# Optimization experiments

Measured on AMD Instinct MI355X. Metric: run time of the kernel, lower is better.

## Reference

```python
import jax, jax.numpy as jnp
import numpy as np

NUM_HEADS = 16

def setup_inputs() -> dict:
    key = jax.random.key(0)
    k1, k2, k3 = jax.random.split(key, 3)
    B, S, D = 2, 2048, 1024
    return {
        "hidden_states": jax.random.normal(k1, (B, S, D), dtype=jnp.float32),
        "W_attn": jax.random.normal(k2, (D, 3 * D), dtype=jnp.float32) * 0.02,
        "b_attn": jnp.zeros((3 * D,), dtype=jnp.float32),
        "W_proj": jax.random.normal(k3, (D, D), dtype=jnp.float32) * 0.02,
        "b_proj": jnp.zeros((D,), dtype=jnp.float32),
    }

def reference(hidden_states, W_attn, b_attn, W_proj, b_proj):
    B, S, D = hidden_states.shape
    H = NUM_HEADS
    hd = D // H
    # qkv projection (Conv1D == addmm): [B,S,3D]
    qkv = hidden_states @ W_attn + b_attn
    q, k, v = jnp.split(qkv, 3, axis=-1)
    # split heads -> [B,H,S,hd]
    def split_heads(t):
        return t.reshape(B, S, H, hd).transpose(0, 2, 1, 3)
    q, k, v = split_heads(q), split_heads(k), split_heads(v)
    # scaled QK^T: [B,H,S,S]
    scores = jnp.einsum('bhqd,bhkd->bhqk', q, k) / jnp.asarray(hd ** 0.5, dtype=q.dtype)
    causal = jnp.tril(jnp.ones((S, S), dtype=bool))
    mask_value = jnp.finfo(scores.dtype).min
    scores = jnp.where(causal, scores, mask_value)
    probs = jax.nn.softmax(scores, axis=-1)  # attn_pdrop=0 -> no dropout
    out = jnp.einsum('bhqk,bhkd->bhqd', probs, v)
    # merge heads -> [B,S,D]
    out = out.transpose(0, 2, 1, 3).reshape(B, S, D)
    out = out @ W_proj + b_proj  # resid_pdrop=0 -> no dropout
    return out
```

## Files before the change

### kernel.cpp

```cpp
#include <hip/hip_runtime.h>
#include <math.h>

typedef __attribute__((ext_vector_type(8))) short bf16x8;
typedef __attribute__((ext_vector_type(4))) short bf16x4;
typedef __attribute__((ext_vector_type(4))) float f32x4;

#define MFMA16(a, b, c) __builtin_amdgcn_mfma_f32_16x16x32_bf16(a, b, c, 0, 0, 0)

#define GLOAD_LDS16(g, l)                                                        \
    __builtin_amdgcn_global_load_lds(                                            \
        (const __attribute__((address_space(1))) void*)(g),                      \
        (__attribute__((address_space(3))) void*)(l), 16, 0, 0)

#define SBAR() __builtin_amdgcn_s_barrier()
#define PRIO(x) __builtin_amdgcn_s_setprio(x)
#define VMW6 asm volatile("s_waitcnt vmcnt(6)" ::: "memory")
#define VMW4 asm volatile("s_waitcnt vmcnt(4)" ::: "memory")
#define VMW2 asm volatile("s_waitcnt vmcnt(2)" ::: "memory")
#define VMW0 asm volatile("s_waitcnt vmcnt(0)" ::: "memory")
#define NOPS ((void)0)

__device__ __forceinline__ short f2bf(float f) {
    union { float f; unsigned u; } x; x.f = f;
    unsigned r = (x.u + 0x7fffu + ((x.u >> 16) & 1u)) >> 16;
    return (short)r;
}

__global__ __launch_bounds__(256) void prep_kernel(
    const float* __restrict__ hs, short* __restrict__ hs_bf,
    const float* __restrict__ Wa, const float* __restrict__ Wp,
    short* __restrict__ WaT, short* __restrict__ WpT) {
    __shared__ float tile[32][33];
    const int bid = blockIdx.x;
    if (bid < 4096) {
        int i = bid * 256 + threadIdx.x;
        float4 v = ((const float4*)hs)[i];
        bf16x4 o;
        o[0] = f2bf(v.x); o[1] = f2bf(v.y); o[2] = f2bf(v.z); o[3] = f2bf(v.w);
        ((bf16x4*)hs_bf)[i] = o;
        return;
    }
    const int xb2 = bid - 4096;
    const int xbb = xb2 & 127;
    const int ky = xb2 >> 7;
    const float* W; short* Wt; int N, xb;
    if (xbb < 96) { W = Wa; Wt = WaT; N = 3072; xb = xbb; }
    else          { W = Wp; Wt = WpT; N = 1024; xb = xbb - 96; }
    const int K = 1024;
    int c = threadIdx.x & 31, r0 = threadIdx.x >> 5;
    int n0 = xb << 5, k0 = ky << 5;
#pragma unroll
    for (int i = 0; i < 4; i++) {
        int r = r0 + i * 8;
        tile[r][c] = W[(long)(k0 + r) * N + n0 + c];
    }
    __syncthreads();
#pragma unroll
    for (int i = 0; i < 4; i++) {
        int r = r0 + i * 8;
        Wt[(long)(n0 + r) * K + k0 + c] = f2bf(tile[c][r]);
    }
}

#define LDA8(IDX) (*(const bf16x8*)&ls[(IDX)])
#define SA(q, k1v, nbv) GLOAD_LDS16(Ags + (size_t)(q) * 65536 + (k1v), &ls[(nbv) + (q) * 4096 + swd])
#define SB(q, k1v, nbv) GLOAD_LDS16(Bgs + (size_t)(q) * 65536 + (k1v), &ls[(nbv) + 32768 + (q) * 4096 + swd])

#define PHASE_MFMA(M0_, M1_, aa0, ba0, aa1, ba1)              \
    PRIO(1);                                                  \
    acc[M0_][0] = MFMA16(aa0, b00, acc[M0_][0]);              \
    acc[M0_][1] = MFMA16(aa0, b10, acc[M0_][1]);              \
    acc[M0_][2] = MFMA16(aa0, b20, acc[M0_][2]);              \
    acc[M0_][3] = MFMA16(aa0, b30, acc[M0_][3]);              \
    acc[M1_][0] = MFMA16(ba0, b00, acc[M1_][0]);              \
    acc[M1_][1] = MFMA16(ba0, b10, acc[M1_][1]);              \
    acc[M1_][2] = MFMA16(ba0, b20, acc[M1_][2]);              \
    acc[M1_][3] = MFMA16(ba0, b30, acc[M1_][3]);              \
    acc[M0_][0] = MFMA16(aa1, b01, acc[M0_][0]);              \
    acc[M0_][1] = MFMA16(aa1, b11, acc[M0_][1]);              \
    acc[M0_][2] = MFMA16(aa1, b21, acc[M0_][2]);              \
    acc[M0_][3] = MFMA16(aa1, b31, acc[M0_][3]);              \
    acc[M1_][0] = MFMA16(ba1, b01, acc[M1_][0]);              \
    acc[M1_][1] = MFMA16(ba1, b11, acc[M1_][1]);              \
    acc[M1_][2] = MFMA16(ba1, b21, acc[M1_][2]);              \
    acc[M1_][3] = MFMA16(ba1, b31, acc[M1_][3]);              \
    PRIO(0);

#define KTILE(T, STG, VMP2, VMTAIL) do {                                              \
    const int cb = ((T) & 1) << 14;                                                   \
    const int nb = cb ^ 16384;                                                        \
    const int k1 = ((T) + 1) << 6;                                                    \
    (void)nb; (void)k1;                                                               \
                                                                    \
    if (STG) { SB(0, k1, nb); SB(1, k1, nb); }                                        \
    const bf16x8 b00 = LDA8(cb + 32768 + bro + sw0);                                  \
    const bf16x8 b01 = LDA8(cb + 32768 + bro + sw1);                                  \
    const bf16x8 b10 = LDA8(cb + 32768 + bro + 1024 + sw0);                           \
    const bf16x8 b11 = LDA8(cb + 32768 + bro + 1024 + sw1);                           \
    const bf16x8 b20 = LDA8(cb + 32768 + bro + 2048 + sw0);                           \
    const bf16x8 b21 = LDA8(cb + 32768 + bro + 2048 + sw1);                           \
    const bf16x8 b30 = LDA8(cb + 32768 + bro + 3072 + sw0);                           \
    const bf16x8 b31 = LDA8(cb + 32768 + bro + 3072 + sw1);                           \
    {                                                                                 \
        bf16x8 x0 = LDA8(cb + aro + sw0), x1 = LDA8(cb + aro + sw1);                  \
        bf16x8 y0 = LDA8(cb + aro + 1024 + sw0), y1 = LDA8(cb + aro + 1024 + sw1);    \
        SBAR();                                                                       \
        PHASE_MFMA(0, 1, x0, y0, x1, y1)                                              \
        SBAR();                                                                       \
    }                                                                                 \
                                                                    \
    if (STG) { SB(2, k1, nb); SB(3, k1, nb); }                                        \
    {                                                                                 \
        bf16x8 x0 = LDA8(cb + aro + 2048 + sw0), x1 = LDA8(cb + aro + 2048 + sw1);    \
        bf16x8 y0 = LDA8(cb + aro + 3072 + sw0), y1 = LDA8(cb + aro + 3072 + sw1);    \
        SBAR();                                                                       \
        PHASE_MFMA(2, 3, x0, y0, x1, y1)                                              \
        SBAR();                                                                       \
    }                                                                                 \
                                                                    \
    VMP2;                                                                             \
    SBAR();                                                                           \
    if (STG) { SA(0, k1, nb); SA(2, k1, nb); }                                        \
    {                                                                                 \
        bf16x8 x0 = LDA8(cb + aro + 4096 + sw0), x1 = LDA8(cb + aro + 4096 + sw1);    \
        bf16x8 y0 = LDA8(cb + aro + 5120 + sw0), y1 = LDA8(cb + aro + 5120 + sw1);    \
        PHASE_MFMA(4, 5, x0, y0, x1, y1)                                              \
        SBAR();                                                                       \
    }                                                                                 \
                                                                    \
    if (STG) { SA(1, k1, nb); SA(3, k1, nb); }                                        \
    {                                                                                 \
        bf16x8 x0 = LDA8(cb + aro + 6144 + sw0), x1 = LDA8(cb + aro + 6144 + sw1);    \
        bf16x8 y0 = LDA8(cb + aro + 7168 + sw0), y1 = LDA8(cb + aro + 7168 + sw1);    \
        SBAR();                                                                       \
        PHASE_MFMA(6, 7, x0, y0, x1, y1)                                              \
        VMTAIL;                                                                       \
        SBAR();                                                                       \
    }                                                                                 \
} while (0)

__global__ __launch_bounds__(512, 2) void gemm_qkv_kernel(
    const short* __restrict__ A, const short* __restrict__ Bt,
    const float* __restrict__ bias,
    short* __restrict__ QK, short* __restrict__ VTb) {
    __shared__ __align__(16) short ls[65536];
    const int tid = threadIdx.x;
    const int lane = tid & 63, l15 = lane & 15, quad = lane >> 4;
    const int w = tid >> 6, wm = w >> 2, wn = w & 3;
    const int m0 = blockIdx.y * 256, n0 = blockIdx.x * 256;
    const int e = l15 & 7;
    const int sgr = (w << 3) + (lane >> 3);
    const int sgc = ((lane & 7) ^ (lane >> 3)) << 3;
    const int swd = w << 9;
    const short* Ags = A + (size_t)(m0 + sgr) * 1024 + sgc;
    const short* Bgs = Bt + (size_t)(n0 + sgr) * 1024 + sgc;
    const int aro = (wm * 128 + l15) << 6;
    const int bro = (wn * 64 + l15) << 6;
    const int sw0 = (quad ^ e) << 3;
    const int sw1 = ((4 + quad) ^ e) << 3;

    f32x4 acc[8][4];
#pragma unroll
    for (int i = 0; i < 8; i++)
#pragma unroll
        for (int j = 0; j < 4; j++) acc[i][j] = (f32x4){0.f, 0.f, 0.f, 0.f};

    SB(0, 0, 0); SB(1, 0, 0); SB(2, 0, 0); SB(3, 0, 0);
    SA(0, 0, 0); SA(2, 0, 0); SA(1, 0, 0); SA(3, 0, 0);
    VMW2;
    SBAR();

#pragma unroll 2
    for (int t = 0; t < 14; ++t) { KTILE(t, 1, VMW4, VMW2); }
    KTILE(14, 1, VMW4, VMW0);
    KTILE(15, 0, VMW0, NOPS);

    __syncthreads();

    if (n0 < 2048) {
        const float scale = (n0 < 1024) ? 0.18033688011112042f : 1.0f;
#pragma unroll
        for (int nt = 0; nt < 4; nt++) {
            const int nn = n0 + wn * 64 + nt * 16 + l15;
            const float bv = bias[nn];
#pragma unroll
            for (int mt = 0; mt < 8; mt++)
#pragma unroll
                for (int r = 0; r < 4; r++) {
                    const int mm = m0 + wm * 128 + mt * 16 + quad * 4 + r;
                    QK[(long)mm * 2048 + nn] = f2bf((acc[mt][nt][r] + bv) * scale);
                }
        }
    } else {
        short* vt = &ls[w * 4352];
        const int hh = ((n0 - 2048) >> 6) + wn;
        const int bb = m0 >> 11;
        const int srow = (m0 & 2047) + wm * 128;
        const int sloc = (lane & 7) << 3;
#pragma unroll
        for (int half = 0; half < 2; half++) {
#pragma unroll
            for (int nt = 0; nt < 4; nt++) {
                const int nn = n0 + wn * 64 + nt * 16 + l15;
                const float bv = bias[nn];
                const int d_ = nt * 16 + l15;
#pragma unroll
                for (int mt = 0; mt < 4; mt++) {
                    const int mtg = half * 4 + mt;
                    bf16x4 pk;
#pragma unroll
                    for (int r = 0; r < 4; r++) pk[r] = f2bf(acc[mtg][nt][r] + bv);
                    *(bf16x4*)&vt[d_ * 68 + mt * 16 + quad * 4] = pk;
                }
            }
#pragma unroll
            for (int i = 0; i < 8; i++) {
                const int d = i * 8 + (lane >> 3);
                bf16x8 vv = *(const bf16x8*)&vt[d * 68 + sloc];
                *(bf16x8*)&VTb[((size_t)(bb * 16 + hh) * 64 + d) * 2048 + srow + half * 64 + sloc] = vv;
            }
        }
    }
}

#define PJ_ISSUE(K0, BB) do {                                                               \
    const int i0 = (w << 2);                                                                \
    GLOAD_LDS16(&Ap[(size_t)((i0 << 3) + lrow) * 1024 + (K0) + lgcol], &ls[(BB) + i0 * 512]);             \
    GLOAD_LDS16(&Ap[(size_t)(((i0 + 1) << 3) + lrow) * 1024 + (K0) + lgcol], &ls[(BB) + (i0 + 1) * 512]); \
    GLOAD_LDS16(&Ap[(size_t)(((i0 + 2) << 3) + lrow) * 1024 + (K0) + lgcol], &ls[(BB) + (i0 + 2) * 512]); \
    GLOAD_LDS16(&Ap[(size_t)(((i0 + 3) << 3) + lrow) * 1024 + (K0) + lgcol], &ls[(BB) + (i0 + 3) * 512]); \
    const int j0 = (w << 1);                                                                \
    GLOAD_LDS16(&Bp[(size_t)((j0 << 3) + lrow) * 1024 + (K0) + lgcol], &ls[(BB) + 8192 + j0 * 512]);      \
    GLOAD_LDS16(&Bp[(size_t)(((j0 + 1) << 3) + lrow) * 1024 + (K0) + lgcol], &ls[(BB) + 8192 + (j0 + 1) * 512]); \
} while (0)

__global__ __launch_bounds__(256, 2) void gemm_proj_kernel(
    const short* __restrict__ A, const short* __restrict__ Bt,
    const float* __restrict__ bias, float* __restrict__ outF) {
    __shared__ __align__(16) short ls[36864];
    const int tid = threadIdx.x;
    const int lane = tid & 63, l15 = lane & 15, quad = lane >> 4, w = tid >> 6;
    const int m0 = blockIdx.y * 128, n0 = blockIdx.x * 64;
    const int e = l15 & 7;
    const int lrow = lane >> 3;
    const int lgcol = ((lane & 7) ^ lrow) << 3;
    const short* Ap = A + (size_t)m0 * 1024;
    const short* Bp = Bt + (size_t)n0 * 1024;

    f32x4 acc[2][4];
#pragma unroll
    for (int i = 0; i < 2; i++)
#pragma unroll
        for (int j = 0; j < 4; j++) acc[i][j] = (f32x4){0.f, 0.f, 0.f, 0.f};

    PJ_ISSUE(0, 0);
    PJ_ISSUE(64, 12288);
    VMW6;
    SBAR();

    int cur = 0;
    for (int t = 0; t < 16; ++t) {
        const int bb = cur * 12288;
        if (t < 14) {
            const int nb2 = (cur == 0) ? 24576 : (cur - 1) * 12288;
            PJ_ISSUE((t + 2) << 6, nb2);
        }
#pragma unroll
        for (int kb = 0; kb < 8; kb += 4) {
            const int sw = (((kb + quad) ^ e) << 3);
            bf16x8 af0 = *(const bf16x8*)&ls[bb + (w * 32 + l15) * 64 + sw];
            bf16x8 af1 = *(const bf16x8*)&ls[bb + (w * 32 + 16 + l15) * 64 + sw];
            bf16x8 bf0 = *(const bf16x8*)&ls[bb + 8192 + (l15) * 64 + sw];
            bf16x8 bf1 = *(const bf16x8*)&ls[bb + 8192 + (16 + l15) * 64 + sw];
            bf16x8 bf2 = *(const bf16x8*)&ls[bb + 8192 + (32 + l15) * 64 + sw];
            bf16x8 bf3 = *(const bf16x8*)&ls[bb + 8192 + (48 + l15) * 64 + sw];
            PRIO(1);
            acc[0][0] = MFMA16(af0, bf0, acc[0][0]);
            acc[0][1] = MFMA16(af0, bf1, acc[0][1]);
            acc[0][2] = MFMA16(af0, bf2, acc[0][2]);
            acc[0][3] = MFMA16(af0, bf3, acc[0][3]);
            acc[1][0] = MFMA16(af1, bf0, acc[1][0]);
            acc[1][1] = MFMA16(af1, bf1, acc[1][1]);
            acc[1][2] = MFMA16(af1, bf2, acc[1][2]);
            acc[1][3] = MFMA16(af1, bf3, acc[1][3]);
            PRIO(0);
        }
        if (t < 14) { VMW6; SBAR(); }
        else if (t == 14) { VMW0; SBAR(); }
        cur = (cur == 2) ? 0 : cur + 1;
    }

#pragma unroll
    for (int nt = 0; nt < 4; nt++) {
        int nn = n0 + nt * 16 + l15;
        float bv = bias[nn];
#pragma unroll
        for (int mt = 0; mt < 2; mt++)
#pragma unroll
            for (int r = 0; r < 4; r++) {
                int mm = m0 + w * 32 + mt * 16 + quad * 4 + r;
                outF[(long)mm * 1024 + nn] = acc[mt][nt][r] + bv;
            }
    }
}

__global__ __launch_bounds__(256, 4) void attn_kernel(
    const short* __restrict__ QK, const short* __restrict__ VT,
    short* __restrict__ Ao) {
    __shared__ __align__(16) short Kt[2][64 * 64];
    __shared__ __align__(16) short Vt[2][64 * 64];
    __shared__ __align__(16) short Pt[4][1024];
    const int tid = threadIdx.x;
    const int lane = tid & 63, l15 = lane & 15, quad = lane >> 4, w = tid >> 6;
    const int bx = blockIdx.x;
    const int p = bx >> 5;
    const int hb = bx & 31;
    const int b = hb >> 4, h = hb & 15;
    const size_t rowbase = (size_t)b * 2048 * 2048 + h * 64;
    const short* Qb = QK + rowbase;
    const short* Kb = QK + rowbase + 1024;
    const short* Vh = VT + (size_t)hb * 64 * 2048;
    short* Pw = &Pt[w][0];
    const int e = l15 & 7;

    const int srow0 = tid >> 3, sc40 = (tid & 7) ^ (srow0 & 7);
    const int srow1 = srow0 + 32, sc41 = (tid & 7) ^ (srow1 & 7);
    const int sdst0 = srow0 * 64 + ((tid & 7) << 3);
    const int sdst1 = srow1 * 64 + ((tid & 7) << 3);

    for (int half = 0; half < 2; half++) {
        const int qt = half ? p : (31 - p);
        const int nc = qt + 1;

        const long qr = (long)(qt * 64 + w * 16 + l15) * 2048;
        bf16x8 qf0 = *(const bf16x8*)&Qb[qr + quad * 8];
        bf16x8 qf1 = *(const bf16x8*)&Qb[qr + 32 + quad * 8];

        float l = 0.f;
        f32x4 o[4];
#pragma unroll
        for (int dt = 0; dt < 4; dt++) o[dt] = (f32x4){0.f, 0.f, 0.f, 0.f};

        *(bf16x8*)&Kt[0][sdst0] = *(const bf16x8*)&Kb[(size_t)srow0 * 2048 + sc40 * 8];
        *(bf16x8*)&Kt[0][sdst1] = *(const bf16x8*)&Kb[(size_t)srow1 * 2048 + sc41 * 8];
        *(bf16x8*)&Vt[0][sdst0] = *(const bf16x8*)&Vh[srow0 * 2048 + sc40 * 8];
        *(bf16x8*)&Vt[0][sdst1] = *(const bf16x8*)&Vh[srow1 * 2048 + sc41 * 8];
        __syncthreads();

        for (int c = 0; c < nc; c++) {
            const short* Kc = &Kt[c & 1][0];
            const short* Vc = &Vt[c & 1][0];
            const bool more = (c + 1 < nc);
            bf16x8 kr0, kr1, vr0, vr1;
            if (more) {
                const int k2 = (c + 1) * 64;
                kr0 = *(const bf16x8*)&Kb[(size_t)(k2 + srow0) * 2048 + sc40 * 8];
                kr1 = *(const bf16x8*)&Kb[(size_t)(k2 + srow1) * 2048 + sc41 * 8];
                vr0 = *(const bf16x8*)&Vh[srow0 * 2048 + k2 + sc40 * 8];
                vr1 = *(const bf16x8*)&Vh[srow1 * 2048 + k2 + sc41 * 8];
            }

            f32x4 s[4];
            PRIO(1);
#pragma unroll
            for (int t = 0; t < 4; t++) {
                bf16x8 k0f = *(const bf16x8*)&Kc[(t * 16 + l15) * 64 + ((quad ^ e) << 3)];
                bf16x8 k1f = *(const bf16x8*)&Kc[(t * 16 + l15) * 64 + (((4 + quad) ^ e) << 3)];
                f32x4 z = (f32x4){0.f, 0.f, 0.f, 0.f};
                z = MFMA16(k0f, qf0, z);
                z = MFMA16(k1f, qf1, z);
                s[t] = z;
            }
            PRIO(0);

            if (c == nc - 1) {
#pragma unroll
                for (int t = 0; t < 4; t++)
#pragma unroll
                    for (int r = 0; r < 4; r++)
                        if (t * 16 + quad * 4 + r > w * 16 + l15) s[t][r] = -INFINITY;
            }

#pragma unroll
            for (int t = 0; t < 4; t++) {
                bf16x4 pw;
#pragma unroll
                for (int r = 0; r < 4; r++) {
                    float pv = __builtin_amdgcn_exp2f(s[t][r]);
                    l += pv;
                    pw[r] = f2bf(pv);
                }
                *(bf16x4*)&Pw[l15 * 64 + (((2 * t + (quad >> 1)) ^ e) << 3) + ((quad & 1) << 2)] = pw;
            }

            bf16x8 pf0 = *(const bf16x8*)&Pw[l15 * 64 + ((quad ^ e) << 3)];
            bf16x8 pf1 = *(const bf16x8*)&Pw[l15 * 64 + (((4 + quad) ^ e) << 3)];
            PRIO(1);
#pragma unroll
            for (int dt = 0; dt < 4; dt++) {
                bf16x8 v0f = *(const bf16x8*)&Vc[(dt * 16 + l15) * 64 + ((quad ^ e) << 3)];
                bf16x8 v1f = *(const bf16x8*)&Vc[(dt * 16 + l15) * 64 + (((4 + quad) ^ e) << 3)];
                o[dt] = MFMA16(v0f, pf0, o[dt]);
                o[dt] = MFMA16(v1f, pf1, o[dt]);
            }
            PRIO(0);

            if (more) {
                short* Kn = &Kt[(c + 1) & 1][0];
                short* Vn = &Vt[(c + 1) & 1][0];
                *(bf16x8*)&Kn[sdst0] = kr0;
                *(bf16x8*)&Kn[sdst1] = kr1;
                *(bf16x8*)&Vn[sdst0] = vr0;
                *(bf16x8*)&Vn[sdst1] = vr1;
            }
            __syncthreads();
        }

        l += __shfl_xor(l, 16);
        l += __shfl_xor(l, 32);
        const float rl = 1.f / l;

        const int qs = qt * 64 + w * 16 + l15;
        const long base = ((long)(b * 2048 + qs)) * 1024 + h * 64;
#pragma unroll
        for (int dt = 0; dt < 4; dt++) {
            bf16x4 wv;
#pragma unroll
            for (int r = 0; r < 4; r++) wv[r] = f2bf(o[dt][r] * rl);
            *(bf16x4*)&Ao[base + dt * 16 + quad * 4] = wv;
        }
    }
}

extern "C" void kernel_launch(void* const* d_in, const int* in_sizes, int n_in,
                              void* d_out, int out_size, void* d_ws, size_t ws_size,
                              hipStream_t stream) {
    const float* hs = (const float*)d_in[0];
    const float* W_attn = (const float*)d_in[1];
    const float* b_attn = (const float*)d_in[2];
    const float* W_proj = (const float*)d_in[3];
    const float* b_proj = (const float*)d_in[4];
    float* out = (float*)d_out;

    const size_t MB = 1024 * 1024;
    char* ws = (char*)d_ws;
    short* hs_bf = (short*)ws;
    short* attn_o = hs_bf;
    short* WaT = (short*)(ws + 8 * MB);
    short* WpT = (short*)(ws + 14 * MB);
    short* QK = (short*)(ws + 16 * MB);
    short* VTb = (short*)(ws + 32 * MB);

    prep_kernel<<<8192, 256, 0, stream>>>(hs, hs_bf, W_attn, W_proj, WaT, WpT);
    gemm_qkv_kernel<<<dim3(12, 16), 512, 0, stream>>>(hs_bf, WaT, b_attn, QK, VTb);
    attn_kernel<<<512, 256, 0, stream>>>(QK, VTb, attn_o);
    gemm_proj_kernel<<<dim3(16, 32), 256, 0, stream>>>(attn_o, WpT, b_proj, out);
}
```

Baseline: 172.5 us.

## Use direct global-to-LDS loads and one query tile per block in attention

The attention kernel now loads K/V tiles with global_load_lds, going straight into shared memory without a register round trip, and waits on vmcnt before the barrier. It also drops the paired heavy/light query-tile loop, so each block handles one query tile and the grid doubles to 1024 blocks, scheduled heaviest first. The s_setprio hints are removed. The aim is lower register pressure and more parallelism, but the paired-tile load balancing is lost and the per-iteration vmcnt(0) wait may expose load latency.

```diff
diff --git a/kernel.cpp b/kernel.cpp
--- a/kernel.cpp
+++ b/kernel.cpp
@@ -313,7 +313,7 @@
     const int tid = threadIdx.x;
     const int lane = tid & 63, l15 = lane & 15, quad = lane >> 4, w = tid >> 6;
     const int bx = blockIdx.x;
-    const int p = bx >> 5;
+    const int qt = 31 - (bx >> 5);
     const int hb = bx & 31;
     const int b = hb >> 4, h = hb & 15;
     const size_t rowbase = (size_t)b * 2048 * 2048 + h * 64;
@@ -323,112 +323,98 @@
     short* Pw = &Pt[w][0];
     const int e = l15 & 7;
 
-    const int srow0 = tid >> 3, sc40 = (tid & 7) ^ (srow0 & 7);
-    const int srow1 = srow0 + 32, sc41 = (tid & 7) ^ (srow1 & 7);
-    const int sdst0 = srow0 * 64 + ((tid & 7) << 3);
-    const int sdst1 = srow1 * 64 + ((tid & 7) << 3);
-
-    for (int half = 0; half < 2; half++) {
-        const int qt = half ? p : (31 - p);
-        const int nc = qt + 1;
-
-        const long qr = (long)(qt * 64 + w * 16 + l15) * 2048;
-        bf16x8 qf0 = *(const bf16x8*)&Qb[qr + quad * 8];
-        bf16x8 qf1 = *(const bf16x8*)&Qb[qr + 32 + quad * 8];
-
-        float l = 0.f;
-        f32x4 o[4];
-#pragma unroll
-        for (int dt = 0; dt < 4; dt++) o[dt] = (f32x4){0.f, 0.f, 0.f, 0.f};
-
-        *(bf16x8*)&Kt[0][sdst0] = *(const bf16x8*)&Kb[(size_t)srow0 * 2048 + sc40 * 8];
-        *(bf16x8*)&Kt[0][sdst1] = *(const bf16x8*)&Kb[(size_t)srow1 * 2048 + sc41 * 8];
-        *(bf16x8*)&Vt[0][sdst0] = *(const bf16x8*)&Vh[srow0 * 2048 + sc40 * 8];
-        *(bf16x8*)&Vt[0][sdst1] = *(const bf16x8*)&Vh[srow1 * 2048 + sc41 * 8];
-        __syncthreads();
-
-        for (int c = 0; c < nc; c++) {
-            const short* Kc = &Kt[c & 1][0];
-            const short* Vc = &Vt[c & 1][0];
-            const bool more = (c + 1 < nc);
-            bf16x8 kr0, kr1, vr0, vr1;
-            if (more) {
-                const int k2 = (c + 1) * 64;
-                kr0 = *(const bf16x8*)&Kb[(size_t)(k2 + srow0) * 2048 + sc40 * 8];
-                kr1 = *(const bf16x8*)&Kb[(size_t)(k2 + srow1) * 2048 + sc41 * 8];
-                vr0 = *(const bf16x8*)&Vh[srow0 * 2048 + k2 + sc40 * 8];
-                vr1 = *(const bf16x8*)&Vh[srow1 * 2048 + k2 + sc41 * 8];
+    const int srow0 = tid >> 3;
+    const int srow1 = srow0 + 32;
+    const int sc4 = (tid & 7) ^ (srow0 & 7);
+    const int wdst = w << 9;
+
+    const long qr = (long)(qt * 64 + w * 16 + l15) * 2048;
+    bf16x8 qf0 = *(const bf16x8*)&Qb[qr + quad * 8];
+    bf16x8 qf1 = *(const bf16x8*)&Qb[qr + 32 + quad * 8];
+
+    float l = 0.f;
+    f32x4 o[4];
+#pragma unroll
+    for (int dt = 0; dt < 4; dt++) o[dt] = (f32x4){0.f, 0.f, 0.f, 0.f};
+
+    const int nc = qt + 1;
+
+    GLOAD_LDS16(&Kb[(size_t)srow0 * 2048 + sc4 * 8], &Kt[0][wdst]);
+    GLOAD_LDS16(&Kb[(size_t)srow1 * 2048 + sc4 * 8], &Kt[0][2048 + wdst]);
+    GLOAD_LDS16(&Vh[srow0 * 2048 + sc4 * 8], &Vt[0][wdst]);
+    GLOAD_LDS16(&Vh[srow1 * 2048 + sc4 * 8], &Vt[0][2048 + wdst]);
+    VMW0;
+    SBAR();
+
+    for (int c = 0; c < nc; c++) {
+        const short* Kc = &Kt[c & 1][0];
+        const short* Vc = &Vt[c & 1][0];
+        if (c + 1 < nc) {
+            const int k2 = (c + 1) * 64;
+            const int nb = (c + 1) & 1;
+            GLOAD_LDS16(&Kb[(size_t)(k2 + srow0) * 2048 + sc4 * 8], &Kt[nb][wdst]);
+            GLOAD_LDS16(&Kb[(size_t)(k2 + srow1) * 2048 + sc4 * 8], &Kt[nb][2048 + wdst]);
+            GLOAD_LDS16(&Vh[srow0 * 2048 + k2 + sc4 * 8], &Vt[nb][wdst]);
+            GLOAD_LDS16(&Vh[srow1 * 2048 + k2 + sc4 * 8], &Vt[nb][2048 + wdst]);
+        }
+
+        f32x4 s[4];
+#pragma unroll
+        for (int t = 0; t < 4; t++) {
+            bf16x8 k0f = *(const bf16x8*)&Kc[(t * 16 + l15) * 64 + ((quad ^ e) << 3)];
+            bf16x8 k1f = *(const bf16x8*)&Kc[(t * 16 + l15) * 64 + (((4 + quad) ^ e) << 3)];
+            f32x4 z = (f32x4){0.f, 0.f, 0.f, 0.f};
+            z = MFMA16(k0f, qf0, z);
+            z = MFMA16(k1f, qf1, z);
+            s[t] = z;
+        }
+
+        if (c == nc - 1) {
+#pragma unroll
+            for (int t = 0; t < 4; t++)
+#pragma unroll
+                for (int r = 0; r < 4; r++)
+                    if (t * 16 + quad * 4 + r > w * 16 + l15) s[t][r] = -INFINITY;
+        }
+
+#pragma unroll
+        for (int t = 0; t < 4; t++) {
+            bf16x4 pw;
+#pragma unroll
+            for (int r = 0; r < 4; r++) {
+                float pv = __builtin_amdgcn_exp2f(s[t][r]);
+                l += pv;
+                pw[r] = f2bf(pv);
             }
-
-            f32x4 s[4];
-            PRIO(1);
-#pragma unroll
-            for (int t = 0; t < 4; t++) {
-                bf16x8 k0f = *(const bf16x8*)&Kc[(t * 16 + l15) * 64 + ((quad ^ e) << 3)];
-                bf16x8 k1f = *(const bf16x8*)&Kc[(t * 16 + l15) * 64 + (((4 + quad) ^ e) << 3)];
-                f32x4 z = (f32x4){0.f, 0.f, 0.f, 0.f};
-                z = MFMA16(k0f, qf0, z);
-                z = MFMA16(k1f, qf1, z);
-                s[t] = z;
-            }
-            PRIO(0);
-
-            if (c == nc - 1) {
-#pragma unroll
-                for (int t = 0; t < 4; t++)
-#pragma unroll
-                    for (int r = 0; r < 4; r++)
-                        if (t * 16 + quad * 4 + r > w * 16 + l15) s[t][r] = -INFINITY;
-            }
-
-#pragma unroll
-            for (int t = 0; t < 4; t++) {
-                bf16x4 pw;
-#pragma unroll
-                for (int r = 0; r < 4; r++) {
-                    float pv = __builtin_amdgcn_exp2f(s[t][r]);
-                    l += pv;
-                    pw[r] = f2bf(pv);
-                }
-                *(bf16x4*)&Pw[l15 * 64 + (((2 * t + (quad >> 1)) ^ e) << 3) + ((quad & 1) << 2)] = pw;
-            }
-
-            bf16x8 pf0 = *(const bf16x8*)&Pw[l15 * 64 + ((quad ^ e) << 3)];
-            bf16x8 pf1 = *(const bf16x8*)&Pw[l15 * 64 + (((4 + quad) ^ e) << 3)];
-            PRIO(1);
-#pragma unroll
-            for (int dt = 0; dt < 4; dt++) {
-                bf16x8 v0f = *(const bf16x8*)&Vc[(dt * 16 + l15) * 64 + ((quad ^ e) << 3)];
-                bf16x8 v1f = *(const bf16x8*)&Vc[(dt * 16 + l15) * 64 + (((4 + quad) ^ e) << 3)];
-                o[dt] = MFMA16(v0f, pf0, o[dt]);
-                o[dt] = MFMA16(v1f, pf1, o[dt]);
-            }
-            PRIO(0);
-
-            if (more) {
-                short* Kn = &Kt[(c + 1) & 1][0];
-                short* Vn = &Vt[(c + 1) & 1][0];
-                *(bf16x8*)&Kn[sdst0] = kr0;
-                *(bf16x8*)&Kn[sdst1] = kr1;
-                *(bf16x8*)&Vn[sdst0] = vr0;
-                *(bf16x8*)&Vn[sdst1] = vr1;
-            }
-            __syncthreads();
-        }
-
-        l += __shfl_xor(l, 16);
-        l += __shfl_xor(l, 32);
-        const float rl = 1.f / l;
-
-        const int qs = qt * 64 + w * 16 + l15;
-        const long base = ((long)(b * 2048 + qs)) * 1024 + h * 64;
+            *(bf16x4*)&Pw[l15 * 64 + (((2 * t + (quad >> 1)) ^ e) << 3) + ((quad & 1) << 2)] = pw;
+        }
+
+        bf16x8 pf0 = *(const bf16x8*)&Pw[l15 * 64 + ((quad ^ e) << 3)];
+        bf16x8 pf1 = *(const bf16x8*)&Pw[l15 * 64 + (((4 + quad) ^ e) << 3)];
 #pragma unroll
         for (int dt = 0; dt < 4; dt++) {
-            bf16x4 wv;
-#pragma unroll
-            for (int r = 0; r < 4; r++) wv[r] = f2bf(o[dt][r] * rl);
-            *(bf16x4*)&Ao[base + dt * 16 + quad * 4] = wv;
-        }
+            bf16x8 v0f = *(const bf16x8*)&Vc[(dt * 16 + l15) * 64 + ((quad ^ e) << 3)];
+            bf16x8 v1f = *(const bf16x8*)&Vc[(dt * 16 + l15) * 64 + (((4 + quad) ^ e) << 3)];
+            o[dt] = MFMA16(v0f, pf0, o[dt]);
+            o[dt] = MFMA16(v1f, pf1, o[dt]);
+        }
+
+        VMW0;
+        SBAR();
+    }
+
+    l += __shfl_xor(l, 16);
+    l += __shfl_xor(l, 32);
+    const float rl = 1.f / l;
+
+    const int qs = qt * 64 + w * 16 + l15;
+    const long base = ((long)(b * 2048 + qs)) * 1024 + h * 64;
+#pragma unroll
+    for (int dt = 0; dt < 4; dt++) {
+        bf16x4 wv;
+#pragma unroll
+        for (int r = 0; r < 4; r++) wv[r] = f2bf(o[dt][r] * rl);
+        *(bf16x4*)&Ao[base + dt * 16 + quad * 4] = wv;
     }
 }
 
@@ -453,6 +439,6 @@
 
     prep_kernel<<<8192, 256, 0, stream>>>(hs, hs_bf, W_attn, W_proj, WaT, WpT);
     gemm_qkv_kernel<<<dim3(12, 16), 512, 0, stream>>>(hs_bf, WaT, b_attn, QK, VTb);
-    attn_kernel<<<512, 256, 0, stream>>>(QK, VTb, attn_o);
+    attn_kernel<<<1024, 256, 0, stream>>>(QK, VTb, attn_o);
     gemm_proj_kernel<<<dim3(16, 32), 256, 0, stream>>>(attn_o, WpT, b_proj, out);
 }
```

After: 167.8 us. 2.7% less time.
